# Optimization experiments

Measured on AMD Instinct MI355X. Metric: run time of the kernel, lower is better.

## Reference

```python
import jax, jax.numpy as jnp
import numpy as np

BANDWIDTH = 1.0  # init arg `bandwidth`
N, V, C = 8, 2048, 64


def setup_inputs() -> dict:
    key = jax.random.key(0)
    k1, k2 = jax.random.split(key)
    x = jax.random.normal(k1, (N, V, C), dtype=jnp.float32)
    # nn.Parameter(torch.rand(V, V)) -> uniform[0,1)
    weight = jax.random.uniform(k2, (V, V), dtype=jnp.float32)
    return {"x": x, "weight": weight}


def _pairwise_l2(x):
    # x: (N, V, C) -> dist[n,i,j] = ||x[n,i] - x[n,j]||_2, without the O(V^2*C) blow-up
    sq = jnp.sum(x * x, axis=-1)                                  # (N, V)
    d2 = sq[:, :, None] + sq[:, None, :] - 2.0 * jnp.einsum('nic,njc->nij', x, x)
    d2 = jnp.maximum(d2, 0.0)
    # safe sqrt: subgradient 0 at 0 (matches torch.norm), avoids NaN grads on the diagonal
    safe = jnp.where(d2 > 0, d2, 1.0)
    return jnp.where(d2 > 0, jnp.sqrt(safe), 0.0)


def reference(x, weight):
    dist = _pairwise_l2(x)                                        # (N, V, V)
    adj = jnp.exp((-0.5 / (BANDWIDTH ** 2)) * dist)               # Gaussian kernel on L2 (not squared)
    adj = jnp.einsum('nij,jk->nik', adj, weight)                  # (N, V, V) @ (V, V)
    return jax.nn.softmax(adj, axis=-1)
```

## Files before the change

### kernel.cpp

```cpp
#include <hip/hip_runtime.h>
#include <hip/hip_bf16.h>
#include <math.h>

#define V 2048
#define C 64
#define NB 8
#define M_TOTAL (NB * V)

typedef __attribute__((ext_vector_type(8))) short bf16x8;
typedef __attribute__((ext_vector_type(4))) float f32x4;

static __device__ __forceinline__ unsigned short f2bf(float f) {
    __hip_bfloat16 h = __float2bfloat16(f);
    return *reinterpret_cast<unsigned short*>(&h);
}

#define GLOAD_LDS16(g, l)                                                        \
    __builtin_amdgcn_global_load_lds((const __attribute__((address_space(1))) void*)(g), \
                                     (__attribute__((address_space(3))) void*)(l), 16, 0, 0)


__global__ __launch_bounds__(256) void q_kernel(const float* __restrict__ x,
                                                float* __restrict__ q) {
    const int gw   = blockIdx.x * 4 + (threadIdx.x >> 6);
    const int lane = threadIdx.x & 63;
    const int lr = lane & 15, lq = lane >> 4;

    const float* rp = x + (size_t)(gw * 16 + lr) * C + lq * 8;
    float4 f0 = *(const float4*)(rp);
    float4 f1 = *(const float4*)(rp + 4);
    float4 f2 = *(const float4*)(rp + 32);
    float4 f3 = *(const float4*)(rp + 36);

    bf16x8 a0, a1;
    a0[0] = (short)f2bf(f0.x); a0[1] = (short)f2bf(f0.y);
    a0[2] = (short)f2bf(f0.z); a0[3] = (short)f2bf(f0.w);
    a0[4] = (short)f2bf(f1.x); a0[5] = (short)f2bf(f1.y);
    a0[6] = (short)f2bf(f1.z); a0[7] = (short)f2bf(f1.w);
    a1[0] = (short)f2bf(f2.x); a1[1] = (short)f2bf(f2.y);
    a1[2] = (short)f2bf(f2.z); a1[3] = (short)f2bf(f2.w);
    a1[4] = (short)f2bf(f3.x); a1[5] = (short)f2bf(f3.y);
    a1[6] = (short)f2bf(f3.z); a1[7] = (short)f2bf(f3.w);

    f32x4 acc = (f32x4){0.f, 0.f, 0.f, 0.f};
    acc = __builtin_amdgcn_mfma_f32_16x16x32_bf16(a0, a0, acc, 0, 0, 0);
    acc = __builtin_amdgcn_mfma_f32_16x16x32_bf16(a1, a1, acc, 0, 0, 0);

    const int r = lr;
    if (lq == (r >> 2)) q[gw * 16 + r] = acc[r & 3];
}

__global__ __launch_bounds__(256) void adj_mfma(const float* __restrict__ x,
                                                const float* __restrict__ q,
                                                unsigned short* __restrict__ adjb) {
    const int n  = blockIdx.z;
    const int i0 = blockIdx.y * 128;
    const int j0 = blockIdx.x * 128;
    const size_t nV = (size_t)n * V;

    __shared__ short Xi[128][72];
    __shared__ short Xj[128][72];
    __shared__ float Qi[128];
    __shared__ float Qj[128];

    const float* xn = x + nV * C;
    const int tid = threadIdx.x;

    for (int idx = tid; idx < 1024; idx += 256) {
        const int row = idx >> 3;
        const int c8  = (idx & 7) * 8;
        float4 ai0 = *(const float4*)(xn + (size_t)(i0 + row) * C + c8);
        float4 ai1 = *(const float4*)(xn + (size_t)(i0 + row) * C + c8 + 4);
        float4 aj0 = *(const float4*)(xn + (size_t)(j0 + row) * C + c8);
        float4 aj1 = *(const float4*)(xn + (size_t)(j0 + row) * C + c8 + 4);
        bf16x8 pi, pj;
        pi[0] = (short)f2bf(ai0.x); pi[1] = (short)f2bf(ai0.y);
        pi[2] = (short)f2bf(ai0.z); pi[3] = (short)f2bf(ai0.w);
        pi[4] = (short)f2bf(ai1.x); pi[5] = (short)f2bf(ai1.y);
        pi[6] = (short)f2bf(ai1.z); pi[7] = (short)f2bf(ai1.w);
        pj[0] = (short)f2bf(aj0.x); pj[1] = (short)f2bf(aj0.y);
        pj[2] = (short)f2bf(aj0.z); pj[3] = (short)f2bf(aj0.w);
        pj[4] = (short)f2bf(aj1.x); pj[5] = (short)f2bf(aj1.y);
        pj[6] = (short)f2bf(aj1.z); pj[7] = (short)f2bf(aj1.w);
        *(bf16x8*)&Xi[row][c8] = pi;
        *(bf16x8*)&Xj[row][c8] = pj;
    }
    if (tid < 128)       Qi[tid]        = q[nV + i0 + tid];
    else                 Qj[tid - 128]  = q[nV + j0 + (tid - 128)];
    __syncthreads();

    const int wid  = tid >> 6;
    const int lane = tid & 63;
    const int wr = wid >> 1, wc = wid & 1;
    const int lr = lane & 15, lq = lane >> 4;

    bf16x8 a[4][2], b[4][2];
#pragma unroll
    for (int m = 0; m < 4; ++m) {
        a[m][0] = *(const bf16x8*)&Xi[wr * 64 + m * 16 + lr][lq * 8];
        a[m][1] = *(const bf16x8*)&Xi[wr * 64 + m * 16 + lr][32 + lq * 8];
    }
#pragma unroll
    for (int nn = 0; nn < 4; ++nn) {
        b[nn][0] = *(const bf16x8*)&Xj[wc * 64 + nn * 16 + lr][lq * 8];
        b[nn][1] = *(const bf16x8*)&Xj[wc * 64 + nn * 16 + lr][32 + lq * 8];
    }

#pragma unroll
    for (int m = 0; m < 4; ++m) {
#pragma unroll
        for (int nn = 0; nn < 4; ++nn) {
            f32x4 g = (f32x4){0.f, 0.f, 0.f, 0.f};
            g = __builtin_amdgcn_mfma_f32_16x16x32_bf16(a[m][0], b[nn][0], g, 0, 0, 0);
            g = __builtin_amdgcn_mfma_f32_16x16x32_bf16(a[m][1], b[nn][1], g, 0, 0, 0);
            const int col_l = wc * 64 + nn * 16 + lr;
            const float qj = Qj[col_l];
#pragma unroll
            for (int r = 0; r < 4; ++r) {
                const int row_l = wr * 64 + m * 16 + lq * 4 + r;
                float d2 = Qi[row_l] + qj - 2.0f * g[r];
                d2 = fmaxf(d2, 0.0f);
                const float e = expf(-0.5f * sqrtf(d2));
                adjb[(nV + i0 + row_l) * V + j0 + col_l] = f2bf(e);
            }
        }
    }
}

__global__ __launch_bounds__(256) void wt_kernel(const float* __restrict__ w,
                                                 unsigned short* __restrict__ wt) {
    __shared__ float tile[64][65];
    const int r0 = blockIdx.y * 64, c0 = blockIdx.x * 64;
    const int tr = threadIdx.x >> 4;
    const int tc4 = (threadIdx.x & 15) << 2;
#pragma unroll
    for (int it = 0; it < 4; ++it) {
        const int r = tr + 16 * it;
        float4 v = *(const float4*)(w + (size_t)(r0 + r) * V + c0 + tc4);
        tile[r][tc4 + 0] = v.x; tile[r][tc4 + 1] = v.y;
        tile[r][tc4 + 2] = v.z; tile[r][tc4 + 3] = v.w;
    }
    __syncthreads();
#pragma unroll
    for (int it = 0; it < 4; ++it) {
        const int cr = tr + 16 * it;
        ushort4 o;
        o.x = f2bf(tile[tc4 + 0][cr]);
        o.y = f2bf(tile[tc4 + 1][cr]);
        o.z = f2bf(tile[tc4 + 2][cr]);
        o.w = f2bf(tile[tc4 + 3][cr]);
        *(ushort4*)(wt + (size_t)(c0 + cr) * V + r0 + tc4) = o;
    }
}

__device__ __forceinline__ void stage_region(char* smem, int regionOff,
                                             const unsigned short* gbase,
                                             int tile, int ks, int tid) {
#pragma unroll
    for (int s = 0; s < 2; ++s) {
        const int off = s * 8192 + tid * 16;
        const int row = off >> 6;
        const int pb  = off & 63;
        const int lb  = pb ^ (((row >> 1) & 3) << 4);
        const unsigned short* g = gbase + (size_t)row * V + tile * 64 + ks * 32 + (lb >> 1);
        GLOAD_LDS16(g, smem + regionOff + off);
    }
}

#define LDS_FRAG(BUF, BOFF, KS, ROW)                                             \
    (*(const bf16x8*)(smem + (BUF) * 65536 + (BOFF) + (KS) * 16384 +             \
                      (ROW) * 64 + (lqb ^ ((((ROW) >> 1) & 3) << 4))))

#define PHASE(BUF, MS, KS, LOADB, STAGE_STMT, WAITV)                             \
    {                                                                            \
        bf16x8 af[4];                                                            \
        _Pragma("unroll") for (int m = 0; m < 4; ++m) {                          \
            const int row = wr128 + ((MS) + m) * 16 + lr;                        \
            af[m] = LDS_FRAG(BUF, 0, KS, row);                                   \
        }                                                                        \
        if (LOADB) {                                                             \
            _Pragma("unroll") for (int n = 0; n < 4; ++n) {                      \
                const int row = wc64 + n * 16 + lr;                              \
                bf[n] = LDS_FRAG(BUF, 32768, KS, row);                           \
            }                                                                    \
        }                                                                        \
        STAGE_STMT;                                                              \
        if (WAITV) {                                                             \
            asm volatile("s_waitcnt vmcnt(6)" ::: "memory");                     \
            __builtin_amdgcn_sched_barrier(0);                                   \
        }                                                                        \
        __builtin_amdgcn_s_barrier();                                            \
        asm volatile("s_waitcnt lgkmcnt(0)" ::: "memory");                       \
        __builtin_amdgcn_sched_barrier(0);                                       \
        __builtin_amdgcn_s_setprio(1);                                           \
        _Pragma("unroll") for (int m = 0; m < 4; ++m)                            \
            _Pragma("unroll") for (int n = 0; n < 4; ++n)                        \
                acc[(MS) + m][n] = __builtin_amdgcn_mfma_f32_16x16x32_bf16(      \
                    af[m], bf[n], acc[(MS) + m][n], 0, 0, 0);                    \
        __builtin_amdgcn_s_setprio(0);                                           \
        __builtin_amdgcn_s_barrier();                                            \
    }

__global__ __launch_bounds__(512, 2) void gemm_8ph(const unsigned short* __restrict__ adjb,
                                                   const unsigned short* __restrict__ wtb,
                                                   float* __restrict__ out) {
    extern __shared__ char smem[];

    const int bid = blockIdx.x;
    const int swz = (bid & 7) * 64 + (bid >> 3);
    const int by = swz >> 3;
    const int bx = swz & 7;
    const int i0 = by * 256;
    const int n0 = bx * 256;

    const int tid  = threadIdx.x;
    const int wid  = tid >> 6;
    const int lane = tid & 63;
    const int wr = wid >> 2, wc = wid & 3;
    const int wr128 = wr * 128, wc64 = wc * 64;
    const int lr = lane & 15, lq = lane >> 4;
    const int lqb = lq * 16;

    const unsigned short* gA = adjb + (size_t)i0 * V;
    const unsigned short* gB = wtb  + (size_t)n0 * V;

    f32x4 acc[8][4];
#pragma unroll
    for (int m = 0; m < 8; ++m)
#pragma unroll
        for (int n = 0; n < 4; ++n) acc[m][n] = (f32x4){0.f, 0.f, 0.f, 0.f};

    stage_region(smem, 32768,         gB, 0, 0, tid);
    stage_region(smem, 0,             gA, 0, 0, tid);
    stage_region(smem, 49152,         gB, 0, 1, tid);
    stage_region(smem, 16384,         gA, 0, 1, tid);
    stage_region(smem, 65536 + 32768, gB, 1, 0, tid);
    stage_region(smem, 65536 + 0,     gA, 1, 0, tid);
    stage_region(smem, 65536 + 49152, gB, 1, 1, tid);
    asm volatile("s_waitcnt vmcnt(6)" ::: "memory");
    __builtin_amdgcn_sched_barrier(0);
    __builtin_amdgcn_s_barrier();

    bf16x8 bf[4];

#pragma unroll 1
    for (int i = 0; i < 16; ++i) {
        const int t1b = 2 * i + 1;
        const int t2  = (2 * i + 2 < 32) ? 2 * i + 2 : 31;
        const int t3  = (2 * i + 3 < 32) ? 2 * i + 3 : 31;

        PHASE(0, 0, 0, true,  stage_region(smem, 65536 + 16384, gA, t1b, 1, tid), false)
        PHASE(0, 4, 0, false, stage_region(smem, 32768,         gB, t2,  0, tid), false)
        PHASE(0, 0, 1, true,  stage_region(smem, 0,             gA, t2,  0, tid), false)
        PHASE(0, 4, 1, false, stage_region(smem, 49152,         gB, t2,  1, tid), true)
        PHASE(1, 0, 0, true,  stage_region(smem, 16384,         gA, t2,  1, tid), false)
        PHASE(1, 4, 0, false, stage_region(smem, 65536 + 32768, gB, t3,  0, tid), false)
        PHASE(1, 0, 1, true,  stage_region(smem, 65536 + 0,     gA, t3,  0, tid), false)
        PHASE(1, 4, 1, false, stage_region(smem, 65536 + 49152, gB, t3,  1, tid), true)
    }

    float* op = out + (size_t)(i0 + wr128) * V + n0 + wc64;
#pragma unroll
    for (int m = 0; m < 8; ++m)
#pragma unroll
        for (int n = 0; n < 4; ++n)
#pragma unroll
            for (int r = 0; r < 4; ++r)
                op[(size_t)(m * 16 + lq * 4 + r) * V + n * 16 + lr] = acc[m][n][r];
}

__global__ __launch_bounds__(256) void gemm_mfma(const unsigned short* __restrict__ adjb,
                                                 const unsigned short* __restrict__ wtb,
                                                 float* __restrict__ out) {
    const int bid = blockIdx.x;
    const int swz = (bid & 7) * 256 + (bid >> 3);
    const int by = swz >> 4;
    const int bx = swz & 15;
    const int i0 = by * 128;
    const int n0 = bx * 128;

    __shared__ alignas(16) unsigned short As[128 * 32];
    __shared__ alignas(16) unsigned short Bs[128 * 32];

    const int tid  = threadIdx.x;
    const int wid  = tid >> 6;
    const int lane = tid & 63;
    const int wr = wid >> 1, wc = wid & 1;
    const int lr = lane & 15, lq = lane >> 4;

    f32x4 acc[4][4];
#pragma unroll
    for (int m = 0; m < 4; ++m)
#pragma unroll
        for (int n = 0; n < 4; ++n) acc[m][n] = (f32x4){0.f, 0.f, 0.f, 0.f};

    const unsigned short* ga = adjb + (size_t)(i0 + (tid >> 2)) * V + (tid & 3) * 8;
    const unsigned short* gb = wtb  + (size_t)(n0 + (tid >> 2)) * V + (tid & 3) * 8;
    unsigned short* lA = &As[tid * 8];
    unsigned short* lB = &Bs[tid * 8];
    const size_t rowskip = (size_t)64 * V;

    for (int kt = 0; kt < 64; ++kt) {
        const int k0 = kt * 32;
        if (kt) __syncthreads();
        GLOAD_LDS16(ga + k0,           lA);
        GLOAD_LDS16(ga + rowskip + k0, lA + 256 * 8);
        GLOAD_LDS16(gb + k0,           lB);
        GLOAD_LDS16(gb + rowskip + k0, lB + 256 * 8);
        __syncthreads();

        bf16x8 a[4], b[4];
#pragma unroll
        for (int m = 0; m < 4; ++m)
            a[m] = *(const bf16x8*)&As[(wr * 64 + m * 16 + lr) * 32 + lq * 8];
#pragma unroll
        for (int n = 0; n < 4; ++n)
            b[n] = *(const bf16x8*)&Bs[(wc * 64 + n * 16 + lr) * 32 + lq * 8];
#pragma unroll
        for (int m = 0; m < 4; ++m)
#pragma unroll
            for (int n = 0; n < 4; ++n)
                acc[m][n] = __builtin_amdgcn_mfma_f32_16x16x32_bf16(a[m], b[n], acc[m][n], 0, 0, 0);
    }

    float* outp = out + (size_t)(i0 + wr * 64) * V + n0 + wc * 64;
#pragma unroll
    for (int m = 0; m < 4; ++m) {
        const int r0 = m * 16 + lq * 4;
#pragma unroll
        for (int n = 0; n < 4; ++n) {
            const int cc = n * 16 + lr;
#pragma unroll
            for (int r = 0; r < 4; ++r)
                outp[(size_t)(r0 + r) * V + cc] = acc[m][n][r];
        }
    }
}


__global__ __launch_bounds__(256) void adj_kernel(const float* __restrict__ x,
                                                  float* __restrict__ adj) {
    const int n  = blockIdx.z;
    const int i0 = blockIdx.y * 64;
    const int j0 = blockIdx.x * 64;

    __shared__ float Xi[64][65];
    __shared__ float Xj[64][65];

    const float* xn = x + (size_t)n * V * C;
    const int tid = threadIdx.x;
    const int lr = tid >> 4;
    const int lc = (tid & 15) << 2;
#pragma unroll
    for (int it = 0; it < 4; ++it) {
        const int r = lr + it * 16;
        float4 vi = *(const float4*)(xn + (size_t)(i0 + r) * C + lc);
        float4 vj = *(const float4*)(xn + (size_t)(j0 + r) * C + lc);
        Xi[r][lc + 0] = vi.x; Xi[r][lc + 1] = vi.y; Xi[r][lc + 2] = vi.z; Xi[r][lc + 3] = vi.w;
        Xj[r][lc + 0] = vj.x; Xj[r][lc + 1] = vj.y; Xj[r][lc + 2] = vj.z; Xj[r][lc + 3] = vj.w;
    }
    __syncthreads();

    const int ti = (tid >> 4) << 2;
    const int tj = (tid & 15) << 2;

    float acc[4][4] = {};
#pragma unroll 4
    for (int c = 0; c < C; ++c) {
        float ai[4], bj[4];
#pragma unroll
        for (int a = 0; a < 4; ++a) ai[a] = Xi[ti + a][c];
#pragma unroll
        for (int b = 0; b < 4; ++b) bj[b] = Xj[tj + b][c];
#pragma unroll
        for (int a = 0; a < 4; ++a)
#pragma unroll
            for (int b = 0; b < 4; ++b) {
                const float d = ai[a] - bj[b];
                acc[a][b] = fmaf(d, d, acc[a][b]);
            }
    }

    float* outb = adj + ((size_t)n * V + i0) * V + j0;
#pragma unroll
    for (int a = 0; a < 4; ++a) {
        float4 o0;
        o0.x = expf(-0.5f * sqrtf(acc[a][0]));
        o0.y = expf(-0.5f * sqrtf(acc[a][1]));
        o0.z = expf(-0.5f * sqrtf(acc[a][2]));
        o0.w = expf(-0.5f * sqrtf(acc[a][3]));
        *(float4*)(outb + (size_t)(ti + a) * V + tj) = o0;
    }
}

__global__ __launch_bounds__(256) void gemm_inplace(float* __restrict__ adjout,
                                                    const float* __restrict__ w) {
    const int n  = blockIdx.y;
    const int i0 = blockIdx.x * 8;

    __shared__ float rows[8][V];

    float* base = adjout + ((size_t)n * V + i0) * V;
    const int tid = threadIdx.x;

    for (int t = tid; t < (8 * V) / 4; t += 256) {
        const int r = t >> 9;
        const int c = (t & 511) << 2;
        float4 v = *(const float4*)(base + (size_t)r * V + c);
        rows[r][c + 0] = v.x; rows[r][c + 1] = v.y; rows[r][c + 2] = v.z; rows[r][c + 3] = v.w;
    }
    __syncthreads();

    float acc[8][8] = {};
    const int k0 = tid << 3;
    const float* wp = w + k0;

    for (int j = 0; j < V; ++j) {
        float a[8];
#pragma unroll
        for (int r = 0; r < 8; ++r) a[r] = rows[r][j];
        const float* wr = wp + (size_t)j * V;
        const float4 w0 = *(const float4*)(wr);
        const float4 w1 = *(const float4*)(wr + 4);
        const float wv[8] = {w0.x, w0.y, w0.z, w0.w, w1.x, w1.y, w1.z, w1.w};
#pragma unroll
        for (int r = 0; r < 8; ++r)
#pragma unroll
            for (int c = 0; c < 8; ++c)
                acc[r][c] = fmaf(a[r], wv[c], acc[r][c]);
    }

#pragma unroll
    for (int r = 0; r < 8; ++r) {
        float4 o0, o1;
        o0.x = acc[r][0]; o0.y = acc[r][1]; o0.z = acc[r][2]; o0.w = acc[r][3];
        o1.x = acc[r][4]; o1.y = acc[r][5]; o1.z = acc[r][6]; o1.w = acc[r][7];
        *(float4*)(base + (size_t)r * V + k0)     = o0;
        *(float4*)(base + (size_t)r * V + k0 + 4) = o1;
    }
}

__global__ __launch_bounds__(256) void softmax_kernel(float* __restrict__ out) {
    const int row  = blockIdx.x * 4 + (threadIdx.x >> 6);
    const int lane = threadIdx.x & 63;
    float* p = out + (size_t)row * V;

    float4 v[8];
#pragma unroll
    for (int s = 0; s < 8; ++s)
        v[s] = *(const float4*)(p + (size_t)(s * 64 + lane) * 4);

    float m = -INFINITY;
#pragma unroll
    for (int s = 0; s < 8; ++s)
        m = fmaxf(m, fmaxf(fmaxf(v[s].x, v[s].y), fmaxf(v[s].z, v[s].w)));
#pragma unroll
    for (int o = 32; o; o >>= 1) m = fmaxf(m, __shfl_xor(m, o));

    float sum = 0.0f;
#pragma unroll
    for (int s = 0; s < 8; ++s) {
        v[s].x = expf(v[s].x - m);
        v[s].y = expf(v[s].y - m);
        v[s].z = expf(v[s].z - m);
        v[s].w = expf(v[s].w - m);
        sum += (v[s].x + v[s].y) + (v[s].z + v[s].w);
    }
#pragma unroll
    for (int o = 32; o; o >>= 1) sum += __shfl_xor(sum, o);

    const float inv = 1.0f / sum;
#pragma unroll
    for (int s = 0; s < 8; ++s) {
        float4 o4;
        o4.x = v[s].x * inv; o4.y = v[s].y * inv;
        o4.z = v[s].z * inv; o4.w = v[s].w * inv;
        *(float4*)(p + (size_t)(s * 64 + lane) * 4) = o4;
    }
}

extern "C" void kernel_launch(void* const* d_in, const int* in_sizes, int n_in,
                              void* d_out, int out_size, void* d_ws, size_t ws_size,
                              hipStream_t stream) {
    const float* x = (const float*)d_in[0];
    const float* w = (const float*)d_in[1];
    float* out = (float*)d_out;

    const size_t adj_elems = (size_t)M_TOTAL * V;
    const size_t need = adj_elems * 2 + (size_t)V * V * 2;

    if (ws_size >= need) {
        unsigned short* adjb = (unsigned short*)d_ws;
        unsigned short* wtb  = adjb + adj_elems;
        float* q = out;

        q_kernel<<<M_TOTAL / 64, 256, 0, stream>>>(x, q);
        adj_mfma<<<dim3(V / 128, V / 128, NB), 256, 0, stream>>>(x, q, adjb);
        wt_kernel<<<dim3(V / 64, V / 64), 256, 0, stream>>>(w, wtb);

        hipError_t attr_ok = hipFuncSetAttribute(
            reinterpret_cast<const void*>(&gemm_8ph),
            hipFuncAttributeMaxDynamicSharedMemorySize, 131072);
        if (attr_ok == hipSuccess) {
            gemm_8ph<<<512, 512, 131072, stream>>>(adjb, wtb, out);
        } else {
            gemm_mfma<<<2048, 256, 0, stream>>>(adjb, wtb, out);
        }
        softmax_kernel<<<(NB * V) / 4, 256, 0, stream>>>(out);
    } else {
        dim3 g1(V / 64, V / 64, NB);
        adj_kernel<<<g1, 256, 0, stream>>>(x, out);
        dim3 g2(V / 8, NB);
        gemm_inplace<<<g2, 256, 0, stream>>>(out, w);
        softmax_kernel<<<(NB * V) / 4, 256, 0, stream>>>(out);
    }
}
```

Baseline: 208.0 us.

## Fuse softmax exp and partial row sums into GEMM epilogue, add normalize pass

The GEMM epilogue now computes exp of each accumulator and stores it as fp16. It also reduces per-row partial sums across lanes and writes them to a small workspace buffer. A new normalize kernel adds the 32 partials per row and scales the fp16 exp values into the fp32 output. This replaces the separate softmax pass over the fp32 GEMM result and is meant to cut memory traffic. The trade-offs are that softmax skips max subtraction (overflow risk for large logits), exp values lose precision in fp16, and the path needs extra workspace.

```diff
diff --git a/kernel.cpp b/kernel.cpp
--- a/kernel.cpp
+++ b/kernel.cpp
@@ -1,5 +1,6 @@
 #include <hip/hip_runtime.h>
 #include <hip/hip_bf16.h>
+#include <hip/hip_fp16.h>
 #include <math.h>
 
 #define V 2048
@@ -13,6 +14,14 @@
 static __device__ __forceinline__ unsigned short f2bf(float f) {
     __hip_bfloat16 h = __float2bfloat16(f);
     return *reinterpret_cast<unsigned short*>(&h);
+}
+static __device__ __forceinline__ unsigned short f2h(float f) {
+    __half h = __float2half(f);
+    return *reinterpret_cast<unsigned short*>(&h);
+}
+static __device__ __forceinline__ float h2f(unsigned short u) {
+    __half h = *reinterpret_cast<__half*>(&u);
+    return __half2float(h);
 }
 
 #define GLOAD_LDS16(g, l)                                                        \
@@ -201,9 +210,12 @@
         __builtin_amdgcn_s_barrier();                                            \
     }
 
+template <int FUSED>
 __global__ __launch_bounds__(512, 2) void gemm_8ph(const unsigned short* __restrict__ adjb,
                                                    const unsigned short* __restrict__ wtb,
-                                                   float* __restrict__ out) {
+                                                   float* __restrict__ out,
+                                                   unsigned short* __restrict__ expw,
+                                                   float* __restrict__ partial) {
     extern __shared__ char smem[];
 
     const int bid = blockIdx.x;
@@ -259,14 +271,71 @@
         PHASE(1, 4, 1, false, stage_region(smem, 65536 + 49152, gB, t3,  1, tid), true)
     }
 
-    float* op = out + (size_t)(i0 + wr128) * V + n0 + wc64;
-#pragma unroll
-    for (int m = 0; m < 8; ++m)
-#pragma unroll
-        for (int n = 0; n < 4; ++n)
-#pragma unroll
-            for (int r = 0; r < 4; ++r)
-                op[(size_t)(m * 16 + lq * 4 + r) * V + n * 16 + lr] = acc[m][n][r];
+    if (FUSED) {
+        unsigned short* ep = expw + (size_t)(i0 + wr128) * V + n0 + wc64;
+        const int slot = bx * 4 + wc;
+#pragma unroll
+        for (int m = 0; m < 8; ++m) {
+            float rp[4] = {0.f, 0.f, 0.f, 0.f};
+#pragma unroll
+            for (int n = 0; n < 4; ++n)
+#pragma unroll
+                for (int r = 0; r < 4; ++r) {
+                    const float e = expf(acc[m][n][r]);
+                    rp[r] += e;
+                    ep[(size_t)(m * 16 + lq * 4 + r) * V + n * 16 + lr] = f2h(e);
+                }
+#pragma unroll
+            for (int r = 0; r < 4; ++r) {
+                rp[r] += __shfl_xor(rp[r], 1);
+                rp[r] += __shfl_xor(rp[r], 2);
+                rp[r] += __shfl_xor(rp[r], 4);
+                rp[r] += __shfl_xor(rp[r], 8);
+            }
+            if (lr == 0) {
+#pragma unroll
+                for (int r = 0; r < 4; ++r)
+                    partial[(size_t)(i0 + wr128 + m * 16 + lq * 4 + r) * 32 + slot] = rp[r];
+            }
+        }
+    } else {
+        float* op = out + (size_t)(i0 + wr128) * V + n0 + wc64;
+#pragma unroll
+        for (int m = 0; m < 8; ++m)
+#pragma unroll
+            for (int n = 0; n < 4; ++n)
+#pragma unroll
+                for (int r = 0; r < 4; ++r)
+                    op[(size_t)(m * 16 + lq * 4 + r) * V + n * 16 + lr] = acc[m][n][r];
+    }
+}
+
+__global__ __launch_bounds__(256) void normalize_kernel(const unsigned short* __restrict__ expw,
+                                                        const float* __restrict__ partial,
+                                                        float* __restrict__ out) {
+    const int row  = blockIdx.x * 4 + (threadIdx.x >> 6);
+    const int lane = threadIdx.x & 63;
+
+    float s = (lane < 32) ? partial[(size_t)row * 32 + lane] : 0.0f;
+#pragma unroll
+    for (int o = 32; o; o >>= 1) s += __shfl_xor(s, o);
+    const float inv = 1.0f / s;
+
+    const unsigned short* ip = expw + (size_t)row * V;
+    float* op = out + (size_t)row * V;
+#pragma unroll
+    for (int t = 0; t < 4; ++t) {
+        const int base = (t * 64 + lane) * 8;
+        ushort4 u0 = *(const ushort4*)(ip + base);
+        ushort4 u1 = *(const ushort4*)(ip + base + 4);
+        float4 o0, o1;
+        o0.x = h2f(u0.x) * inv; o0.y = h2f(u0.y) * inv;
+        o0.z = h2f(u0.z) * inv; o0.w = h2f(u0.w) * inv;
+        o1.x = h2f(u1.x) * inv; o1.y = h2f(u1.y) * inv;
+        o1.z = h2f(u1.z) * inv; o1.w = h2f(u1.w) * inv;
+        *(float4*)(op + base)     = o0;
+        *(float4*)(op + base + 4) = o1;
+    }
 }
 
 __global__ __launch_bounds__(256) void gemm_mfma(const unsigned short* __restrict__ adjb,
@@ -487,7 +556,11 @@
     float* out = (float*)d_out;
 
     const size_t adj_elems = (size_t)M_TOTAL * V;
-    const size_t need = adj_elems * 2 + (size_t)V * V * 2;
+    const size_t wt_elems  = (size_t)V * V;
+    const size_t need      = (adj_elems + wt_elems) * 2;
+    const size_t exp_off   = need;
+    const size_t part_off  = exp_off + adj_elems * 2;
+    const size_t need_big  = part_off + (size_t)M_TOTAL * 32 * 4;
 
     if (ws_size >= need) {
         unsigned short* adjb = (unsigned short*)d_ws;
@@ -498,11 +571,23 @@
         adj_mfma<<<dim3(V / 128, V / 128, NB), 256, 0, stream>>>(x, q, adjb);
         wt_kernel<<<dim3(V / 64, V / 64), 256, 0, stream>>>(w, wtb);
 
-        hipError_t attr_ok = hipFuncSetAttribute(
-            reinterpret_cast<const void*>(&gemm_8ph),
+        if (ws_size >= need_big) {
+            unsigned short* expw = (unsigned short*)((char*)d_ws + exp_off);
+            float* partial       = (float*)((char*)d_ws + part_off);
+            hipError_t ok = hipFuncSetAttribute(
+                reinterpret_cast<const void*>(&gemm_8ph<1>),
+                hipFuncAttributeMaxDynamicSharedMemorySize, 131072);
+            if (ok == hipSuccess) {
+                gemm_8ph<1><<<512, 512, 131072, stream>>>(adjb, wtb, out, expw, partial);
+                normalize_kernel<<<M_TOTAL / 4, 256, 0, stream>>>(expw, partial, out);
+                return;
+            }
+        }
+        hipError_t ok = hipFuncSetAttribute(
+            reinterpret_cast<const void*>(&gemm_8ph<0>),
             hipFuncAttributeMaxDynamicSharedMemorySize, 131072);
-        if (attr_ok == hipSuccess) {
-            gemm_8ph<<<512, 512, 131072, stream>>>(adjb, wtb, out);
+        if (ok == hipSuccess) {
+            gemm_8ph<0><<<512, 512, 131072, stream>>>(adjb, wtb, out, nullptr, nullptr);
         } else {
             gemm_mfma<<<2048, 256, 0, stream>>>(adjb, wtb, out);
         }
```

Result: no change. 211.4 us (+1.6%).
